# Optimization experiments

Measured on AMD Instinct MI355X. Metric: run time of the kernel, lower is better.

Reference implementation:

```python
import jax, jax.numpy as jnp
import numpy as np

DEPTH = 18  # leaves at level DEPTH; internal nodes = 2**DEPTH - 1
INPUT_SIZE = 128
HIDDEN = 128  # H; internal nn.LSTM runs with hidden size 2*H


def setup_inputs() -> dict:
    key = jax.random.key(0)
    k_emb, k_wih, k_whh, k_bih, k_bhh = jax.random.split(key, 5)
    n_internal = 2 ** DEPTH - 1
    H2 = 2 * HIDDEN
    s = 1.0 / np.sqrt(H2)  # torch nn.LSTM init scale
    return {
        "embeddings": jax.random.normal(k_emb, (n_internal, INPUT_SIZE), jnp.float32),
        "W_ih": jax.random.uniform(k_wih, (4 * H2, INPUT_SIZE), jnp.float32, -s, s),
        "W_hh": jax.random.uniform(k_whh, (4 * H2, H2), jnp.float32, -s, s),
        "b_ih": jax.random.uniform(k_bih, (4 * H2,), jnp.float32, -s, s),
        "b_hh": jax.random.uniform(k_bhh, (4 * H2,), jnp.float32, -s, s),
    }


def _lstm_cell(x, h0, c0, W_ih, W_hh, b_ih, b_hh):
    # single-timestep LSTM with PyTorch gate order (i, f, g, o)
    gates = x @ W_ih.T + b_ih + h0 @ W_hh.T + b_hh  # [n, 4*2H]
    i, f, g, o = jnp.split(gates, 4, axis=-1)
    c = jax.nn.sigmoid(f) * c0 + jax.nn.sigmoid(i) * jnp.tanh(g)
    h = jax.nn.sigmoid(o) * jnpp_tanh(c) if False else jax.nn.sigmoid(o) * jnp.tanh(c)
    return h, c


def reference(embeddings, W_ih, W_hh, b_ih, b_hh):
    H = W_hh.shape[1] // 2
    n_internal = embeddings.shape[0]
    depth = int(round(np.log2(n_internal + 1)))
    n_leaves = n_internal + 1
    # leaf nodes (a is None / b is None): zero hidden and cell of size H
    h = jnp.zeros((n_leaves, H), embeddings.dtype)
    c = jnp.zeros((n_leaves, H), embeddings.dtype)
    # bottom-up over levels; level d holds heap indices [2^d - 1, 2^{d+1} - 1)
    for d in range(depth - 1, -1, -1):
        n = 2 ** d
        x = embeddings[n - 1: 2 * n - 1]           # [n, input_size]
        # children of node k in level d are nodes 2k, 2k+1 in level d+1,
        # so the concat cat((a.hidden, b.hidden), dim=1) is a reshape
        h0 = h.reshape(n, 2 * H)                   # [n, 2H]
        c0 = c.reshape(n, 2 * H)
        h2, c2 = _lstm_cell(x, h0, c0, W_ih, W_hh, b_ih, b_hh)
        # keep only the first H units, as in v[:, :hidden_size]
        h, c = h2[:, :H], c2[:, :H]
    # root state: hidden and cell, each [1, H]
    return jnp.concatenate([h, c], axis=-1)       # [1, 2H]
```

## Files before the change

### kernel.cpp

```cpp
#include <hip/hip_runtime.h>


typedef _Float16 f16;
typedef f16 f16x8 __attribute__((ext_vector_type(8)));
typedef float f32x4 __attribute__((ext_vector_type(4)));

#define MAGIC 0xC0FFEEu
#define LOG2E 1.44269504f
#define RING 6

#define GCNT(x)  ((x) * 32)
#define TOTALI   256
#define MAGICI   257
#define DONEI    258
#define XARR(x)  (320 + (x) * 32)
#define GBARI    576
#define FBARI    608

__device__ __forceinline__ float sigf(float x) {
    return __builtin_amdgcn_rcpf(1.f + __builtin_amdgcn_exp2f(-x * LOG2E));
}
__device__ __forceinline__ float tanh_fast(float x) {
    return 1.f - 2.f * __builtin_amdgcn_rcpf(1.f + __builtin_amdgcn_exp2f(2.f * x * LOG2E));
}

__device__ __forceinline__ void load_lds_16(const void* g, void* l) {
    __builtin_amdgcn_global_load_lds(
        (const __attribute__((address_space(1))) unsigned int*)g,
        (__attribute__((address_space(3))) unsigned int*)l, 16, 0, 0);
}

__global__ __launch_bounds__(256) void pack_weights(
    const float* __restrict__ W_ih, const float* __restrict__ W_hh,
    const float* __restrict__ b_ih, const float* __restrict__ b_hh,
    f16* __restrict__ Bp, float* __restrict__ biasP)
{
    int idx = blockIdx.x * 256 + threadIdx.x;
    if (idx < 196608) {
        int by = idx / 24576;
        int r = idx - by * 24576;
        int kci = r / 2048;
        int r2 = r & 2047;
        int kq = r2 >> 9;
        int r3 = r2 & 511;
        int c = r3 >> 3;
        int k8 = r3 & 7;
        int g = c >> 4, jl = c & 15;
        int rOrig = g * 256 + by * 16 + jl;
        int kk = kci * 32 + kq * 8 + k8;
        float w = (kk < 128) ? W_ih[(size_t)rOrig * 128 + kk]
                             : W_hh[(size_t)rOrig * 256 + (kk - 128)];
        Bp[idx] = (f16)w;
    }
    if (idx < 512) {
        int by = idx >> 6, c = idx & 63;
        int g = c >> 4, jl = c & 15;
        int rOrig = g * 256 + by * 16 + jl;
        biasP[idx] = b_ih[rOrig] + b_hh[rOrig];
    }
}

__global__ __launch_bounds__(256) void emb_cvt(
    const float* __restrict__ emb, f16* __restrict__ embH)
{
    int i = blockIdx.x * 256 + threadIdx.x;
    if (i < 4194288) {
        const float4 a = *(const float4*)(emb + (size_t)i * 8);
        const float4 b = *(const float4*)(emb + (size_t)i * 8 + 4);
        f16x8 r;
        r[0] = (f16)a.x; r[1] = (f16)a.y; r[2] = (f16)a.z; r[3] = (f16)a.w;
        r[4] = (f16)b.x; r[5] = (f16)b.y; r[6] = (f16)b.z; r[7] = (f16)b.w;
        *(f16x8*)(embH + (size_t)i * 8) = r;
    }
}

__device__ __forceinline__ f16* hLvl(char* H, int d) {
    return (f16*)(H + (size_t)256u * ((1u << 18) - (1u << (d + 1))));
}
__device__ __forceinline__ float* cLvl(char* C, int d) {
    return (float*)(C + (size_t)256u * ((1u << 18) - (1u << (d + 1))));
}

template <int AP>
__device__ __forceinline__ f16x8 loadA2(
    const f16* __restrict__ embH, const f16* __restrict__ h_in,
    int n, int row, int kci, int kq)
{
    f16x8 r;
    if (kci < 4) {
        r = *(const f16x8*)(embH + (size_t)(n - 1 + row) * 128 + kci * 32 + kq * 8);
    } else if (AP == 2) {
        int base = (kci - 4) * 32;
        int par = base >> 7;
        int cb = base & 127;
        int pl = (cb >> 4) + (kq >> 1);
        int off = (kq & 1) * 8;
        r = *(const f16x8*)(h_in + ((size_t)pl * 2 * n + (size_t)par * n + row) * 16 + off);
    } else {
        r = *(const f16x8*)(h_in + (size_t)row * 256 + (kci - 4) * 32 + kq * 8);
    }
    return r;
}

template <int NCH, int CLAMP, int AP, int OP>
__device__ __forceinline__ void tile_compute(
    const f16* __restrict__ embH, const f16* __restrict__ Bs,
    int n, int row0, int rlimit, int l15, int kq, int j, int by,
    float bi, float bfv, float bg, float bo,
    const f16* __restrict__ h_in, const float* __restrict__ c_in,
    f16* __restrict__ h_out, float* __restrict__ c_out,
    float* __restrict__ root_out)
{
    f32x4 acc[4][4];
    #pragma unroll
    for (int a = 0; a < 4; ++a)
        #pragma unroll
        for (int b = 0; b < 4; ++b) acc[a][b] = (f32x4)0.f;

    int rowm[4];
    #pragma unroll
    for (int mi = 0; mi < 4; ++mi) {
        int rr = row0 + mi * 16 + l15;
        rowm[mi] = CLAMP ? ((rr < rlimit) ? rr : (rlimit - 1)) : rr;
    }

    float cpre[4][4];
    if (NCH == 12) {
        #pragma unroll
        for (int mi = 0; mi < 4; ++mi) {
            #pragma unroll
            for (int r = 0; r < 4; ++r) {
                int row = row0 + mi * 16 + kq * 4 + r;
                int rc = CLAMP ? ((row < rlimit) ? row : (rlimit - 1)) : row;
                cpre[mi][r] = (AP == 2) ? c_in[((size_t)by * n + rc) * 16 + l15]
                                        : c_in[(size_t)rc * 128 + j];
            }
        }
    }

    f16x8 af[RING][4];
    #pragma unroll
    for (int pk = 0; pk < RING; ++pk) {
        if (pk < NCH) {
            #pragma unroll
            for (int mi = 0; mi < 4; ++mi)
                af[pk][mi] = loadA2<AP>(embH, h_in, n, rowm[mi], pk, kq);
        }
    }

    #pragma unroll
    for (int kci = 0; kci < NCH; ++kci) {
        const int sl = kci % RING;
        f16x8 bf[4];
        #pragma unroll
        for (int g = 0; g < 4; ++g)
            bf[g] = *(const f16x8*)&Bs[((kci * 4 + kq) * 64 + g * 16 + l15) * 8];
        f16x8 a0 = af[sl][0], a1 = af[sl][1], a2 = af[sl][2], a3 = af[sl][3];
        if (kci + RING < NCH) {
            #pragma unroll
            for (int mi = 0; mi < 4; ++mi)
                af[sl][mi] = loadA2<AP>(embH, h_in, n, rowm[mi], kci + RING, kq);
        }
        #pragma unroll
        for (int g = 0; g < 4; ++g) {
            acc[0][g] = __builtin_amdgcn_mfma_f32_16x16x32_f16(a0, bf[g], acc[0][g], 0, 0, 0);
            acc[1][g] = __builtin_amdgcn_mfma_f32_16x16x32_f16(a1, bf[g], acc[1][g], 0, 0, 0);
            acc[2][g] = __builtin_amdgcn_mfma_f32_16x16x32_f16(a2, bf[g], acc[2][g], 0, 0, 0);
            acc[3][g] = __builtin_amdgcn_mfma_f32_16x16x32_f16(a3, bf[g], acc[3][g], 0, 0, 0);
        }
    }

    #pragma unroll
    for (int mi = 0; mi < 4; ++mi) {
        #pragma unroll
        for (int r = 0; r < 4; ++r) {
            int row = row0 + mi * 16 + kq * 4 + r;
            if (!CLAMP || row < rlimit) {
                float gi = acc[mi][0][r] + bi;
                float gf = acc[mi][1][r] + bfv;
                float gg = acc[mi][2][r] + bg;
                float go = acc[mi][3][r] + bo;
                float cl = (NCH == 4) ? 0.f : cpre[mi][r];
                float cn = sigf(gf) * cl + sigf(gi) * tanh_fast(gg);
                float hn = sigf(go) * tanh_fast(cn);
                if (root_out) {
                    root_out[j] = hn;
                    root_out[128 + j] = cn;
                } else if (OP) {
                    h_out[((size_t)by * n + (size_t)(row & 1) * (n >> 1) + (row >> 1)) * 16 + l15] = (f16)hn;
                    if (!(row & 1))
                        c_out[((size_t)by * (n >> 1) + (row >> 1)) * 16 + l15] = cn;
                } else {
                    h_out[(size_t)row * 128 + j] = (f16)hn;
                    if (!(row & 1))
                        c_out[(size_t)(row >> 1) * 128 + j] = cn;
                }
            }
        }
    }
}

__device__ __forceinline__ void stage_chunk(
    const f16* __restrict__ embH, const f16* __restrict__ h_in,
    char* __restrict__ AsW, int buf, int kci, int n, int row0,
    int lane, int gsrc, int srow)
{
    char* dst = AsW + buf * 4096;
    if (kci < 4) {
        const char* eb = (const char*)embH + ((size_t)(n - 1) + row0) * 256 + kci * 64 + gsrc * 16;
        #pragma unroll
        for (int t = 0; t < 4; ++t)
            load_lds_16(eb + ((size_t)(t * 16 + srow)) * 256, dst + t * 1024);
    } else {
        int k0 = (kci - 4) * 32;
        int par = k0 >> 7;
        int cb = k0 & 127;
        int p = (cb >> 4) + (gsrc >> 1);
        const char* hb = (const char*)h_in
            + ((size_t)p * 2 * n + (size_t)par * n + row0) * 32 + (gsrc & 1) * 16;
        #pragma unroll
        for (int t = 0; t < 4; ++t)
            load_lds_16(hb + ((size_t)(t * 16 + srow)) * 32, dst + t * 1024);
    }
}

template <int NCH>
__device__ __forceinline__ void tile_staged(
    const f16* __restrict__ embH, const f16* __restrict__ Bs,
    char* __restrict__ AsW,
    int n, int row0, int lane, int l15, int kq, int j, int by,
    float bi, float bfv, float bg, float bo,
    const f16* __restrict__ h_in, const float* __restrict__ c_in,
    f16* __restrict__ h_out, float* __restrict__ c_out)
{
    const int gsrc = (lane & 3) ^ ((lane >> 3) & 3);
    const int srow = lane >> 2;
    const int gsel = kq ^ ((l15 >> 1) & 3);

    f32x4 acc[4][4];
    #pragma unroll
    for (int a = 0; a < 4; ++a)
        #pragma unroll
        for (int b = 0; b < 4; ++b) acc[a][b] = (f32x4)0.f;

    float cpre[4][4];
    if (NCH == 12) {
        #pragma unroll
        for (int mi = 0; mi < 4; ++mi) {
            #pragma unroll
            for (int r = 0; r < 4; ++r) {
                int row = row0 + mi * 16 + kq * 4 + r;
                cpre[mi][r] = c_in[((size_t)by * n + row) * 16 + l15];
            }
        }
    }

    stage_chunk(embH, h_in, AsW, 0, 0, n, row0, lane, gsrc, srow);
    stage_chunk(embH, h_in, AsW, 1, 1, n, row0, lane, gsrc, srow);

    #pragma unroll
    for (int kci = 0; kci < NCH; ++kci) {
        if (kci + 1 < NCH) asm volatile("s_waitcnt vmcnt(4)" ::: "memory");
        else               asm volatile("s_waitcnt vmcnt(0)" ::: "memory");
        __builtin_amdgcn_sched_barrier(0);

        const f16* slab = (const f16*)(AsW + (kci & 1) * 4096);
        f16x8 a0 = *(const f16x8*)&slab[(0 * 16 + l15) * 32 + gsel * 8];
        f16x8 a1 = *(const f16x8*)&slab[(1 * 16 + l15) * 32 + gsel * 8];
        f16x8 a2 = *(const f16x8*)&slab[(2 * 16 + l15) * 32 + gsel * 8];
        f16x8 a3 = *(const f16x8*)&slab[(3 * 16 + l15) * 32 + gsel * 8];
        f16x8 bf[4];
        #pragma unroll
        for (int g = 0; g < 4; ++g)
            bf[g] = *(const f16x8*)&Bs[((kci * 4 + kq) * 64 + g * 16 + l15) * 8];

        #pragma unroll
        for (int g = 0; g < 4; ++g) {
            acc[0][g] = __builtin_amdgcn_mfma_f32_16x16x32_f16(a0, bf[g], acc[0][g], 0, 0, 0);
            acc[1][g] = __builtin_amdgcn_mfma_f32_16x16x32_f16(a1, bf[g], acc[1][g], 0, 0, 0);
            acc[2][g] = __builtin_amdgcn_mfma_f32_16x16x32_f16(a2, bf[g], acc[2][g], 0, 0, 0);
            acc[3][g] = __builtin_amdgcn_mfma_f32_16x16x32_f16(a3, bf[g], acc[3][g], 0, 0, 0);
        }

        if (kci + 2 < NCH) {
            asm volatile("s_waitcnt lgkmcnt(0)" ::: "memory");
            __builtin_amdgcn_sched_barrier(0);
            stage_chunk(embH, h_in, AsW, kci & 1, kci + 2, n, row0, lane, gsrc, srow);
        }
    }

    #pragma unroll
    for (int mi = 0; mi < 4; ++mi) {
        #pragma unroll
        for (int r = 0; r < 4; ++r) {
            int row = row0 + mi * 16 + kq * 4 + r;
            float gi = acc[mi][0][r] + bi;
            float gf = acc[mi][1][r] + bfv;
            float gg = acc[mi][2][r] + bg;
            float go = acc[mi][3][r] + bo;
            float cl = (NCH == 4) ? 0.f : cpre[mi][r];
            float cn = sigf(gf) * cl + sigf(gi) * tanh_fast(gg);
            float hn = sigf(go) * tanh_fast(cn);
            h_out[((size_t)by * n + (size_t)(row & 1) * (n >> 1) + (row >> 1)) * 16 + l15] = (f16)hn;
            if (!(row & 1))
                c_out[((size_t)by * (n >> 1) + (row >> 1)) * 16 + l15] = cn;
        }
    }
}

__device__ __forceinline__ void gbar(unsigned* sync, unsigned xcc,
                                     unsigned phase, unsigned Gx) {
    __syncthreads();
    if (threadIdx.x == 0) {
        unsigned old = __hip_atomic_fetch_add(&sync[XARR(xcc)], 1u,
                                              __ATOMIC_RELAXED, __HIP_MEMORY_SCOPE_AGENT);
        if (old == phase * Gx - 1u)
            __hip_atomic_fetch_add(&sync[GBARI], 1u,
                                   __ATOMIC_RELAXED, __HIP_MEMORY_SCOPE_AGENT);
        while (__hip_atomic_load(&sync[GBARI], __ATOMIC_RELAXED,
                                 __HIP_MEMORY_SCOPE_AGENT) < phase * 8u)
            __builtin_amdgcn_s_sleep(32);
        asm volatile("buffer_inv sc0" ::: "memory");
    }
    __syncthreads();
}

__global__ __launch_bounds__(256, 2) void mega(
    const f16* __restrict__ embH,
    const f16* __restrict__ Bp, const float* __restrict__ biasP,
    char* __restrict__ H, char* __restrict__ C,
    float* __restrict__ root_out, unsigned* __restrict__ sync)
{
    __shared__ __align__(16) f16 Bs[24576];
    __shared__ __align__(16) f16 As[4][2][2048];
    unsigned* meta = (unsigned*)&As[0][0][0];

    const int tid = threadIdx.x;
    const int lane = tid & 63;
    const int w = tid >> 6;
    const int l15 = lane & 15;
    const int kq = lane >> 4;

    unsigned xcc;
    asm volatile("s_getreg_b32 %0, hwreg(HW_REG_XCC_ID)" : "=s"(xcc));
    xcc &= 7u;

    if (blockIdx.x == 0 && tid == 0) {
        for (int x = 0; x < 8; ++x) {
            __hip_atomic_store(&sync[GCNT(x)], 0u, __ATOMIC_RELAXED, __HIP_MEMORY_SCOPE_AGENT);
            __hip_atomic_store(&sync[XARR(x)], 0u, __ATOMIC_RELAXED, __HIP_MEMORY_SCOPE_AGENT);
        }
        __hip_atomic_store(&sync[TOTALI], 0u, __ATOMIC_RELAXED, __HIP_MEMORY_SCOPE_AGENT);
        __hip_atomic_store(&sync[DONEI], 0u, __ATOMIC_RELAXED, __HIP_MEMORY_SCOPE_AGENT);
        __hip_atomic_store(&sync[GBARI], 0u, __ATOMIC_RELAXED, __HIP_MEMORY_SCOPE_AGENT);
        __hip_atomic_store(&sync[FBARI], 0u, __ATOMIC_RELAXED, __HIP_MEMORY_SCOPE_AGENT);
        __hip_atomic_store(&sync[MAGICI], MAGIC, __ATOMIC_RELEASE, __HIP_MEMORY_SCOPE_AGENT);
    }
    if (tid == 0) {
        while (__hip_atomic_load(&sync[MAGICI], __ATOMIC_RELAXED,
                                 __HIP_MEMORY_SCOPE_AGENT) != MAGIC)
            __builtin_amdgcn_s_sleep(32);
        unsigned r = __hip_atomic_fetch_add(&sync[GCNT(xcc)], 1u,
                                            __ATOMIC_RELAXED, __HIP_MEMORY_SCOPE_AGENT);
        asm volatile("s_waitcnt vmcnt(0)" ::: "memory");
        __hip_atomic_fetch_add(&sync[TOTALI], 1u,
                               __ATOMIC_RELAXED, __HIP_MEMORY_SCOPE_AGENT);
        while (__hip_atomic_load(&sync[TOTALI], __ATOMIC_RELAXED,
                                 __HIP_MEMORY_SCOPE_AGENT) < 512u)
            __builtin_amdgcn_s_sleep(32);
        meta[0] = r;
        meta[1] = __hip_atomic_load(&sync[GCNT(xcc)], __ATOMIC_RELAXED,
                                    __HIP_MEMORY_SCOPE_AGENT);
    }
    __syncthreads();
    const unsigned rank = meta[0];
    const unsigned Gx = meta[1];
    const int by = (int)(rank & 7u);
    const int strm = (int)(rank >> 3);
    const int nstr = (int)((Gx - (unsigned)by + 7u) >> 3);
    __syncthreads();

    {
        const char* gB = (const char*)(Bp + (size_t)by * 24576);
        char* lB = (char*)Bs;
        #pragma unroll
        for (int i = 0; i < 12; ++i)
            load_lds_16(gB + ((size_t)(i * 256 + tid)) * 16,
                        lB + ((size_t)(i * 256 + w * 64)) * 16);
    }
    __syncthreads();

    const int j = by * 16 + l15;
    const float bi = biasP[by * 64 + 0 + l15];
    const float bfv = biasP[by * 64 + 16 + l15];
    const float bg = biasP[by * 64 + 32 + l15];
    const float bo = biasP[by * 64 + 48 + l15];
    char* AsW = (char*)&As[w][0][0];

    unsigned phase = 0;
    for (int d = 17; d >= 3; --d) {
        const int n = 1 << d;
        const int chunk = n >> 3;
        const int base = (int)xcc * chunk;
        const f16* h_in = hLvl(H, d + 1 < 18 ? d + 1 : 17);
        const float* c_in = cLvl(C, d + 1 < 18 ? d + 1 : 17);
        f16* h_out = hLvl(H, d);
        float* c_out = cLvl(C, d);

        if (d == 17) {
            for (int t = strm; t < 64; t += nstr) {
                int row0 = base + t * 256 + w * 64;
                tile_staged<4>(embH, Bs, AsW, n, row0, lane, l15, kq, j, by,
                               bi, bfv, bg, bo, h_in, c_in, h_out, c_out);
            }
        } else if (d >= 11) {
            const int T = 1 << (d - 11);
            for (int t = strm; t < T; t += nstr) {
                int row0 = base + t * 256 + w * 64;
                tile_staged<12>(embH, Bs, AsW, n, row0, lane, l15, kq, j, by,
                                bi, bfv, bg, bo, h_in, c_in, h_out, c_out);
            }
        } else if (d >= 5) {
            if (strm == 0 && w * 64 < chunk) {
                int row0 = base + w * 64;
                tile_compute<12, 1, 2, 1>(embH, Bs, n, row0, base + chunk, l15, kq, j, by,
                                          bi, bfv, bg, bo, h_in, c_in, h_out, c_out, nullptr);
            }
        } else if (d == 4) {
            if (strm == 0 && w * 64 < chunk) {
                int row0 = base + w * 64;
                tile_compute<12, 1, 2, 0>(embH, Bs, n, row0, base + chunk, l15, kq, j, by,
                                          bi, bfv, bg, bo, h_in, c_in, h_out, c_out, nullptr);
            }
        } else {
            if (strm == 0 && w * 64 < chunk) {
                int row0 = base + w * 64;
                tile_compute<12, 1, 0, 0>(embH, Bs, n, row0, base + chunk, l15, kq, j, by,
                                          bi, bfv, bg, bo, h_in, c_in, h_out, c_out, nullptr);
            }
        }

        ++phase;
        gbar(sync, xcc, phase, Gx);
    }

    if (rank == 0 && tid == 0) {
        __threadfence();
        __hip_atomic_fetch_add(&sync[DONEI], 1u,
                               __ATOMIC_RELAXED, __HIP_MEMORY_SCOPE_AGENT);
    }

    const bool fin = (xcc == 0u) && (rank < 8u);
    if (!fin) return;

    if (tid == 0) {
        while (__hip_atomic_load(&sync[DONEI], __ATOMIC_RELAXED,
                                 __HIP_MEMORY_SCOPE_AGENT) < 8u)
            __builtin_amdgcn_s_sleep(32);
        __threadfence();
    }
    __syncthreads();

    unsigned fphase = 0;
    for (int d = 2; d >= 0; --d) {
        const int n = 1 << d;
        const f16* h_in = hLvl(H, d + 1);
        const float* c_in = cLvl(C, d + 1);
        f16* h_out = hLvl(H, d);
        float* c_out = cLvl(C, d);
        if (w == 0)
            tile_compute<12, 1, 0, 0>(embH, Bs, n, 0, n, l15, kq, j, by,
                                      bi, bfv, bg, bo, h_in, c_in, h_out, c_out,
                                      (d == 0) ? (float*)root_out : nullptr);
        if (d > 0) {
            ++fphase;
            __syncthreads();
            if (tid == 0) {
                __hip_atomic_fetch_add(&sync[FBARI], 1u,
                                       __ATOMIC_RELAXED, __HIP_MEMORY_SCOPE_AGENT);
                while (__hip_atomic_load(&sync[FBARI], __ATOMIC_RELAXED,
                                         __HIP_MEMORY_SCOPE_AGENT) < fphase * 8u)
                    __builtin_amdgcn_s_sleep(4);
                asm volatile("buffer_inv sc0" ::: "memory");
            }
            __syncthreads();
        }
    }
}

extern "C" void kernel_launch(void* const* d_in, const int* in_sizes, int n_in,
                              void* d_out, int out_size, void* d_ws, size_t ws_size,
                              hipStream_t stream) {
    const float* emb  = (const float*)d_in[0];
    const float* W_ih = (const float*)d_in[1];
    const float* W_hh = (const float*)d_in[2];
    const float* b_ih = (const float*)d_in[3];
    const float* b_hh = (const float*)d_in[4];

    char* wsb = (char*)d_ws;
    f16*   Bp    = (f16*)wsb;
    float* biasP = (float*)(wsb + 393216);
    unsigned* syncp = (unsigned*)(wsb + 397312);
    f16* embH = (f16*)(wsb + 1048576);
    char* H = wsb + 1048576 + 67108864;
    char* C = wsb + 1048576 + 2 * 67108864;
    if (ws_size < 1048576 + 3 * 67108864) return;

    pack_weights<<<768, 256, 0, stream>>>(W_ih, W_hh, b_ih, b_hh, Bp, biasP);
    emb_cvt<<<16384, 256, 0, stream>>>(emb, (f16*)embH);
    mega<<<512, 256, 0, stream>>>(embH, Bp, biasP, H, C, (float*)d_out, syncp);
}
```

Measured before the change: 461.5 us.

## Use 768-thread blocks with per-wave tile loop and cross-tile prefetch

The persistent kernel goes from 512 blocks of 256 threads to 256 blocks of 768 threads (12 waves each, 12 LDS staging slabs), so each block loads the shared weight slab once for three times as many waves. Tiles are now handed out per wave rather than per 4-wave group. The next tile's c values and first two A chunks are prefetched while the current tile finishes, and the LDS reads are issued before the next chunk's stage. The aim is to cut redundant weight loading and pipeline bubbles between tiles, at the cost of larger blocks, higher LDS use and fewer blocks in the grid barrier. Occupancy may drop and the lower levels may now leave waves idle.

```diff
diff --git a/kernel.cpp b/kernel.cpp
--- a/kernel.cpp
+++ b/kernel.cpp
@@ -203,7 +203,7 @@
 __device__ __forceinline__ void stage_chunk(
     const f16* __restrict__ embH, const f16* __restrict__ h_in,
     char* __restrict__ AsW, int buf, int kci, int n, int row0,
-    int lane, int gsrc, int srow)
+    int gsrc, int srow)
 {
     char* dst = AsW + buf * 4096;
     if (kci < 4) {
@@ -225,86 +225,105 @@
 }
 
 template <int NCH>
-__device__ __forceinline__ void tile_staged(
+__device__ __forceinline__ void run_level(
     const f16* __restrict__ embH, const f16* __restrict__ Bs,
     char* __restrict__ AsW,
-    int n, int row0, int lane, int l15, int kq, int j, int by,
+    int n, int base, int U, int ws, int NWS,
+    int l15, int kq, int gsel, int gsrc, int srow, int by,
     float bi, float bfv, float bg, float bo,
     const f16* __restrict__ h_in, const float* __restrict__ c_in,
     f16* __restrict__ h_out, float* __restrict__ c_out)
 {
-    const int gsrc = (lane & 3) ^ ((lane >> 3) & 3);
-    const int srow = lane >> 2;
-    const int gsel = kq ^ ((l15 >> 1) & 3);
-
-    f32x4 acc[4][4];
-    #pragma unroll
-    for (int a = 0; a < 4; ++a)
-        #pragma unroll
-        for (int b = 0; b < 4; ++b) acc[a][b] = (f32x4)0.f;
+    int u = ws;
+    if (u >= U) return;
+    int row0 = base + u * 64;
 
     float cpre[4][4];
     if (NCH == 12) {
         #pragma unroll
+        for (int mi = 0; mi < 4; ++mi)
+            #pragma unroll
+            for (int r = 0; r < 4; ++r)
+                cpre[mi][r] = c_in[((size_t)by * n + (row0 + mi * 16 + kq * 4 + r)) * 16 + l15];
+    }
+    stage_chunk(embH, h_in, AsW, 0, 0, n, row0, gsrc, srow);
+    stage_chunk(embH, h_in, AsW, 1, 1, n, row0, gsrc, srow);
+
+    while (true) {
+        const int un = u + NWS;
+        const bool more = (un < U);
+        const int nrow0 = base + un * 64;
+
+        f32x4 acc[4][4];
+        #pragma unroll
+        for (int a = 0; a < 4; ++a)
+            #pragma unroll
+            for (int b = 0; b < 4; ++b) acc[a][b] = (f32x4)0.f;
+
+        #pragma unroll
+        for (int kci = 0; kci < NCH; ++kci) {
+            if (kci < NCH - 1) asm volatile("s_waitcnt vmcnt(4)" ::: "memory");
+            else               asm volatile("s_waitcnt vmcnt(0)" ::: "memory");
+            __builtin_amdgcn_sched_barrier(0);
+
+            const f16* slab = (const f16*)(AsW + (kci & 1) * 4096);
+            f16x8 a0 = *(const f16x8*)&slab[(0 * 16 + l15) * 32 + gsel * 8];
+            f16x8 a1 = *(const f16x8*)&slab[(1 * 16 + l15) * 32 + gsel * 8];
+            f16x8 a2 = *(const f16x8*)&slab[(2 * 16 + l15) * 32 + gsel * 8];
+            f16x8 a3 = *(const f16x8*)&slab[(3 * 16 + l15) * 32 + gsel * 8];
+            f16x8 bf[4];
+            #pragma unroll
+            for (int g = 0; g < 4; ++g)
+                bf[g] = *(const f16x8*)&Bs[((kci * 4 + kq) * 64 + g * 16 + l15) * 8];
+
+            if (kci <= NCH - 3) {
+                asm volatile("s_waitcnt lgkmcnt(0)" ::: "memory");
+                __builtin_amdgcn_sched_barrier(0);
+                stage_chunk(embH, h_in, AsW, kci & 1, kci + 2, n, row0, gsrc, srow);
+            }
+
+            #pragma unroll
+            for (int g = 0; g < 4; ++g) {
+                acc[0][g] = __builtin_amdgcn_mfma_f32_16x16x32_f16(a0, bf[g], acc[0][g], 0, 0, 0);
+                acc[1][g] = __builtin_amdgcn_mfma_f32_16x16x32_f16(a1, bf[g], acc[1][g], 0, 0, 0);
+                acc[2][g] = __builtin_amdgcn_mfma_f32_16x16x32_f16(a2, bf[g], acc[2][g], 0, 0, 0);
+                acc[3][g] = __builtin_amdgcn_mfma_f32_16x16x32_f16(a3, bf[g], acc[3][g], 0, 0, 0);
+            }
+        }
+
+        #pragma unroll
         for (int mi = 0; mi < 4; ++mi) {
             #pragma unroll
             for (int r = 0; r < 4; ++r) {
                 int row = row0 + mi * 16 + kq * 4 + r;
-                cpre[mi][r] = c_in[((size_t)by * n + row) * 16 + l15];
-            }
-        }
-    }
-
-    stage_chunk(embH, h_in, AsW, 0, 0, n, row0, lane, gsrc, srow);
-    stage_chunk(embH, h_in, AsW, 1, 1, n, row0, lane, gsrc, srow);
-
-    #pragma unroll
-    for (int kci = 0; kci < NCH; ++kci) {
-        if (kci + 1 < NCH) asm volatile("s_waitcnt vmcnt(4)" ::: "memory");
-        else               asm volatile("s_waitcnt vmcnt(0)" ::: "memory");
+                float gi = acc[mi][0][r] + bi;
+                float gf = acc[mi][1][r] + bfv;
+                float gg = acc[mi][2][r] + bg;
+                float go = acc[mi][3][r] + bo;
+                float cl = (NCH == 4) ? 0.f : cpre[mi][r];
+                float cn = sigf(gf) * cl + sigf(gi) * tanh_fast(gg);
+                float hn = sigf(go) * tanh_fast(cn);
+                h_out[((size_t)by * n + (size_t)(row & 1) * (n >> 1) + (row >> 1)) * 16 + l15] = (f16)hn;
+                if (!(row & 1))
+                    c_out[((size_t)by * (n >> 1) + (row >> 1)) * 16 + l15] = cn;
+            }
+        }
+
+        if (!more) break;
+
+        if (NCH == 12) {
+            #pragma unroll
+            for (int mi = 0; mi < 4; ++mi)
+                #pragma unroll
+                for (int r = 0; r < 4; ++r)
+                    cpre[mi][r] = c_in[((size_t)by * n + (nrow0 + mi * 16 + kq * 4 + r)) * 16 + l15];
+        }
+        asm volatile("s_waitcnt lgkmcnt(0)" ::: "memory");
         __builtin_amdgcn_sched_barrier(0);
-
-        const f16* slab = (const f16*)(AsW + (kci & 1) * 4096);
-        f16x8 a0 = *(const f16x8*)&slab[(0 * 16 + l15) * 32 + gsel * 8];
-        f16x8 a1 = *(const f16x8*)&slab[(1 * 16 + l15) * 32 + gsel * 8];
-        f16x8 a2 = *(const f16x8*)&slab[(2 * 16 + l15) * 32 + gsel * 8];
-        f16x8 a3 = *(const f16x8*)&slab[(3 * 16 + l15) * 32 + gsel * 8];
-        f16x8 bf[4];
-        #pragma unroll
-        for (int g = 0; g < 4; ++g)
-            bf[g] = *(const f16x8*)&Bs[((kci * 4 + kq) * 64 + g * 16 + l15) * 8];
-
-        #pragma unroll
-        for (int g = 0; g < 4; ++g) {
-            acc[0][g] = __builtin_amdgcn_mfma_f32_16x16x32_f16(a0, bf[g], acc[0][g], 0, 0, 0);
-            acc[1][g] = __builtin_amdgcn_mfma_f32_16x16x32_f16(a1, bf[g], acc[1][g], 0, 0, 0);
-            acc[2][g] = __builtin_amdgcn_mfma_f32_16x16x32_f16(a2, bf[g], acc[2][g], 0, 0, 0);
-            acc[3][g] = __builtin_amdgcn_mfma_f32_16x16x32_f16(a3, bf[g], acc[3][g], 0, 0, 0);
-        }
-
-        if (kci + 2 < NCH) {
-            asm volatile("s_waitcnt lgkmcnt(0)" ::: "memory");
-            __builtin_amdgcn_sched_barrier(0);
-            stage_chunk(embH, h_in, AsW, kci & 1, kci + 2, n, row0, lane, gsrc, srow);
-        }
-    }
-
-    #pragma unroll
-    for (int mi = 0; mi < 4; ++mi) {
-        #pragma unroll
-        for (int r = 0; r < 4; ++r) {
-            int row = row0 + mi * 16 + kq * 4 + r;
-            float gi = acc[mi][0][r] + bi;
-            float gf = acc[mi][1][r] + bfv;
-            float gg = acc[mi][2][r] + bg;
-            float go = acc[mi][3][r] + bo;
-            float cl = (NCH == 4) ? 0.f : cpre[mi][r];
-            float cn = sigf(gf) * cl + sigf(gi) * tanh_fast(gg);
-            float hn = sigf(go) * tanh_fast(cn);
-            h_out[((size_t)by * n + (size_t)(row & 1) * (n >> 1) + (row >> 1)) * 16 + l15] = (f16)hn;
-            if (!(row & 1))
-                c_out[((size_t)by * (n >> 1) + (row >> 1)) * 16 + l15] = cn;
-        }
+        stage_chunk(embH, h_in, AsW, 0, 0, n, nrow0, gsrc, srow);
+        stage_chunk(embH, h_in, AsW, 1, 1, n, nrow0, gsrc, srow);
+
+        u = un; row0 = nrow0;
     }
 }
 
@@ -325,14 +344,14 @@
     __syncthreads();
 }
 
-__global__ __launch_bounds__(256, 2) void mega(
+__global__ __launch_bounds__(768, 3) void mega(
     const f16* __restrict__ embH,
     const f16* __restrict__ Bp, const float* __restrict__ biasP,
     char* __restrict__ H, char* __restrict__ C,
     float* __restrict__ root_out, unsigned* __restrict__ sync)
 {
     __shared__ __align__(16) f16 Bs[24576];
-    __shared__ __align__(16) f16 As[4][2][2048];
+    __shared__ __align__(16) f16 As[12][2][2048];
     unsigned* meta = (unsigned*)&As[0][0][0];
 
     const int tid = threadIdx.x;
@@ -340,6 +359,9 @@
     const int w = tid >> 6;
     const int l15 = lane & 15;
     const int kq = lane >> 4;
+    const int gsrc = (lane & 3) ^ ((lane >> 3) & 3);
+    const int srow = lane >> 2;
+    const int gsel = kq ^ ((l15 >> 1) & 3);
 
     unsigned xcc;
     asm volatile("s_getreg_b32 %0, hwreg(HW_REG_XCC_ID)" : "=s"(xcc));
@@ -366,7 +388,7 @@
         __hip_atomic_fetch_add(&sync[TOTALI], 1u,
                                __ATOMIC_RELAXED, __HIP_MEMORY_SCOPE_AGENT);
         while (__hip_atomic_load(&sync[TOTALI], __ATOMIC_RELAXED,
-                                 __HIP_MEMORY_SCOPE_AGENT) < 512u)
+                                 __HIP_MEMORY_SCOPE_AGENT) < 256u)
             __builtin_amdgcn_s_sleep(32);
         meta[0] = r;
         meta[1] = __hip_atomic_load(&sync[GCNT(xcc)], __ATOMIC_RELAXED,
@@ -384,9 +406,9 @@
         const char* gB = (const char*)(Bp + (size_t)by * 24576);
         char* lB = (char*)Bs;
         #pragma unroll
-        for (int i = 0; i < 12; ++i)
-            load_lds_16(gB + ((size_t)(i * 256 + tid)) * 16,
-                        lB + ((size_t)(i * 256 + w * 64)) * 16);
+        for (int i = 0; i < 4; ++i)
+            load_lds_16(gB + ((size_t)(i * 768 + tid)) * 16,
+                        lB + ((size_t)(i * 768 + w * 64)) * 16);
     }
     __syncthreads();
 
@@ -396,6 +418,9 @@
     const float bg = biasP[by * 64 + 32 + l15];
     const float bo = biasP[by * 64 + 48 + l15];
     char* AsW = (char*)&As[w][0][0];
+
+    const int ws = strm * 12 + w;
+    const int NWS = nstr * 12;
 
     unsigned phase = 0;
     for (int d = 17; d >= 3; --d) {
@@ -408,18 +433,13 @@
         float* c_out = cLvl(C, d);
 
         if (d == 17) {
-            for (int t = strm; t < 64; t += nstr) {
-                int row0 = base + t * 256 + w * 64;
-                tile_staged<4>(embH, Bs, AsW, n, row0, lane, l15, kq, j, by,
-                               bi, bfv, bg, bo, h_in, c_in, h_out, c_out);
-            }
+            run_level<4>(embH, Bs, AsW, n, base, chunk >> 6, ws, NWS,
+                         l15, kq, gsel, gsrc, srow, by, bi, bfv, bg, bo,
+                         h_in, c_in, h_out, c_out);
         } else if (d >= 11) {
-            const int T = 1 << (d - 11);
-            for (int t = strm; t < T; t += nstr) {
-                int row0 = base + t * 256 + w * 64;
-                tile_staged<12>(embH, Bs, AsW, n, row0, lane, l15, kq, j, by,
-                                bi, bfv, bg, bo, h_in, c_in, h_out, c_out);
-            }
+            run_level<12>(embH, Bs, AsW, n, base, chunk >> 6, ws, NWS,
+                          l15, kq, gsel, gsrc, srow, by, bi, bfv, bg, bo,
+                          h_in, c_in, h_out, c_out);
         } else if (d >= 5) {
             if (strm == 0 && w * 64 < chunk) {
                 int row0 = base + w * 64;
@@ -508,5 +528,5 @@
 
     pack_weights<<<768, 256, 0, stream>>>(W_ih, W_hh, b_ih, b_hh, Bp, biasP);
     emb_cvt<<<16384, 256, 0, stream>>>(emb, (f16*)embH);
-    mega<<<512, 256, 0, stream>>>(embH, Bp, biasP, H, C, (float*)d_out, syncp);
-}
+    mega<<<256, 768, 0, stream>>>(embH, Bp, biasP, H, C, (float*)d_out, syncp);
+}
```

Measured after the change: 561.8 us. +21.7%, slower.
